# Kernel optimization log

Measured on AMD Instinct MI355X. Metric: run time of the kernel, lower is better.

Reference implementation:

```python
import jax, jax.numpy as jnp
import numpy as np

B, N, M, D = 8, 4096, 4096, 2


def setup_inputs() -> dict:
    key = jax.random.key(0)
    k1, k2, k3, k4 = jax.random.split(key, 4)
    return {
        "predicted_coords": jax.random.normal(k1, (B, N, D), dtype=jnp.float32),
        "predicted_points": jax.random.randint(k2, (B,), N // 2, N + 1, dtype=jnp.int32),
        "target_coords": jax.random.normal(k3, (B, M, D), dtype=jnp.float32),
        "target_points": jax.random.randint(k4, (B,), M // 2, M + 1, dtype=jnp.int32),
    }


def reference(predicted_coords, predicted_points, target_coords, target_points):
    # predicted_coords: [B, N, D], target_coords: [B, M, D]
    # predicted_points / target_points: [B] valid counts
    n = predicted_coords.shape[1]
    d = predicted_coords.shape[2]

    # points_loss = MSE(pred_counts/N, target_counts/N) over the batch
    points_loss = jnp.mean(
        (predicted_points.astype(jnp.float32) / n - target_points.astype(jnp.float32) / n) ** 2
    )

    # Batched 1-NN: squared pairwise distances [B, N, M], invalid targets masked to +inf.
    # (argmin of squared Euclidean == argmin of Euclidean, matching KDTree k=1.)
    d2 = jnp.sum((predicted_coords[:, :, None, :] - target_coords[:, None, :, :]) ** 2, axis=-1)
    tmask = jnp.arange(target_coords.shape[1])[None, :] < target_points[:, None]  # [B, M]
    d2 = jnp.where(tmask[:, None, :], d2, jnp.inf)
    idx = jnp.argmin(d2, axis=-1)  # [B, N]

    # Matched targets are detached in the original (numpy round-trip) -> stop_gradient.
    matched = jax.lax.stop_gradient(
        jnp.take_along_axis(target_coords, idx[:, :, None], axis=1)
    )  # [B, N, D]

    sq = jnp.sum((predicted_coords - matched) ** 2, axis=-1)  # [B, N]
    pmask = jnp.arange(predicted_coords.shape[1])[None, :] < predicted_points[:, None]  # [B, N]
    # Per-sample MSE over valid pred points (mean over count*D elements), then mean over batch.
    denom = predicted_points.astype(jnp.float32) * d
    coord_loss = jnp.mean(jnp.sum(jnp.where(pmask, sq, 0.0), axis=-1) / denom)

    total_loss = coord_loss + 0.1 * points_loss
    return (total_loss, coord_loss, points_loss)
```

## Files before the change

kernel.cpp:

```cpp
#include <hip/hip_runtime.h>
#include <math.h>

#define NB 8
#define NPTS 4096
#define MPTS 4096
#define CHUNK 64
#define NCHUNK (NPTS / CHUNK)
#define NWAVE 8
#define TQ (MPTS / NWAVE)

__device__ __forceinline__ float waveReduceSum(float v) {
#pragma unroll
    for (int off = 32; off > 0; off >>= 1)
        v += __shfl_down(v, off, 64);
    return v;
}

__global__ __launch_bounds__(NWAVE * 64) void nn_kernel(
    const float2* __restrict__ pred,
    const int* __restrict__ pcounts,
    const float2* __restrict__ tgt,
    const int* __restrict__ tcounts,
    float* __restrict__ partials)
{
    __shared__ float sx[MPTS];
    __shared__ float sy[MPTS];
    __shared__ float sc[MPTS];
    __shared__ float mnw[NWAVE][CHUNK];

    const int g = blockIdx.x;
    const int b = g >> 6;
    const int c = g & (NCHUNK - 1);
    const int w = threadIdx.x >> 6;
    const int lane = threadIdx.x & 63;

    const int tcount = tcounts[b];
    const int tstart = w * TQ;

    const float2* tsrc = tgt + (size_t)b * MPTS + tstart;
#pragma unroll
    for (int i = 0; i < TQ / 64; ++i) {
        float2 t = tsrc[i * 64 + lane];
        int idx = tstart + i * 64 + lane;
        sx[idx] = -2.0f * t.x;
        sy[idx] = -2.0f * t.y;
        sc[idx] = fmaf(t.x, t.x, t.y * t.y);
    }

    const float2 p = pred[(size_t)b * NPTS + c * CHUNK + lane];

    int tloc = min(tcount - tstart, TQ);
    if (tloc < 0) tloc = 0;

    float m0 = INFINITY, m1 = INFINITY, m2 = INFINITY, m3 = INFINITY;
    const float4* x4 = (const float4*)&sx[tstart];
    const float4* y4 = (const float4*)&sy[tstart];
    const float4* c4 = (const float4*)&sc[tstart];
    const int nt4 = tloc >> 2;
    for (int i = 0; i < nt4; ++i) {
        float4 xv = x4[i], yv = y4[i], cv = c4[i];
        m0 = fminf(m0, fmaf(p.y, yv.x, fmaf(p.x, xv.x, cv.x)));
        m1 = fminf(m1, fmaf(p.y, yv.y, fmaf(p.x, xv.y, cv.y)));
        m2 = fminf(m2, fmaf(p.y, yv.z, fmaf(p.x, xv.z, cv.z)));
        m3 = fminf(m3, fmaf(p.y, yv.w, fmaf(p.x, xv.w, cv.w)));
    }
    for (int m = nt4 * 4; m < tloc; ++m) {
        float v = fmaf(p.y, sy[tstart + m], fmaf(p.x, sx[tstart + m], sc[tstart + m]));
        m0 = fminf(m0, v);
    }
    mnw[w][lane] = fminf(fminf(m0, m1), fminf(m2, m3));
    __syncthreads();

    if (w == 0) {
        float mn = mnw[0][lane];
#pragma unroll
        for (int j = 1; j < NWAVE; ++j) mn = fminf(mn, mnw[j][lane]);
        float pp = fmaf(p.x, p.x, p.y * p.y);
        float v = (c * CHUNK + lane < pcounts[b]) ? (mn + pp) : 0.0f;
        v = waveReduceSum(v);
        if (lane == 0) partials[g] = v;
    }
}

__global__ __launch_bounds__(512) void final_kernel(
    const float* __restrict__ partials,
    const int* __restrict__ pcounts,
    const int* __restrict__ tcounts,
    float* __restrict__ out)
{
    __shared__ float bs[NB];
    const int w = threadIdx.x >> 6;
    const int lane = threadIdx.x & 63;
    float v = partials[w * NCHUNK + lane];
    v = waveReduceSum(v);
    if (lane == 0) bs[w] = v;
    __syncthreads();
    if (threadIdx.x == 0) {
        float coord = 0.0f, pts = 0.0f;
        for (int b = 0; b < NB; ++b) {
            coord += bs[b] / ((float)pcounts[b] * 2.0f);
            float d = ((float)pcounts[b] - (float)tcounts[b]) / (float)NPTS;
            pts += d * d;
        }
        coord *= (1.0f / NB);
        pts *= (1.0f / NB);
        out[0] = coord + 0.1f * pts;
        out[1] = coord;
        out[2] = pts;
    }
}

extern "C" void kernel_launch(void* const* d_in, const int* in_sizes, int n_in,
                              void* d_out, int out_size, void* d_ws, size_t ws_size,
                              hipStream_t stream) {
    const float2* pred    = (const float2*)d_in[0];
    const int*    pcounts = (const int*)d_in[1];
    const float2* tgt     = (const float2*)d_in[2];
    const int*    tcounts = (const int*)d_in[3];
    float* out = (float*)d_out;

    float* partials = (float*)d_ws;

    nn_kernel<<<NB * NCHUNK, NWAVE * 64, 0, stream>>>(
        pred, pcounts, tgt, tcounts, partials);
    final_kernel<<<1, 512, 0, stream>>>(partials, pcounts, tcounts, out);
}
```

Baseline: 20.33 us.

## Process two predictions per lane with packed FP32 math and 1024-thread blocks

Restructures the nearest-neighbour kernel so each lane handles two predicted points, reusing every loaded target pair. Inner-loop arithmetic uses v_pk_fma/v_pk_mul and v_min3. The target-norm array is no longer precomputed in shared memory; norms are recomputed per target, trading extra FMAs for less LDS traffic. Blocks grow to 1024 threads in 16 waves, halving the block count to 256, and the target load becomes vectorised float4. The final reduction is simplified to a single wave with shuffles.

```diff
diff --git a/kernel.cpp b/kernel.cpp
--- a/kernel.cpp
+++ b/kernel.cpp
@@ -4,10 +4,32 @@
 #define NB 8
 #define NPTS 4096
 #define MPTS 4096
-#define CHUNK 64
-#define NCHUNK (NPTS / CHUNK)
-#define NWAVE 8
-#define TQ (MPTS / NWAVE)
+#define BN (NB * NPTS)
+#define K1_THREADS 1024
+#define K1_WAVES 16
+#define SLICE (MPTS / K1_WAVES)
+#define P 2
+#define PPB (64 * P)
+#define NBLK (BN / PPB)
+#define BPB (NPTS / PPB)
+
+typedef float v2f __attribute__((ext_vector_type(2)));
+
+static __device__ __forceinline__ v2f pk_fma(v2f a, v2f b, v2f c) {
+    v2f d;
+    asm("v_pk_fma_f32 %0, %1, %2, %3" : "=v"(d) : "v"(a), "v"(b), "v"(c));
+    return d;
+}
+static __device__ __forceinline__ v2f pk_mul(v2f a, v2f b) {
+    v2f d;
+    asm("v_pk_mul_f32 %0, %1, %2" : "=v"(d) : "v"(a), "v"(b));
+    return d;
+}
+static __device__ __forceinline__ float min3f(float a, float b, float c) {
+    float d;
+    asm("v_min3_f32 %0, %1, %2, %3" : "=v"(d) : "v"(a), "v"(b), "v"(c));
+    return d;
+}
 
 __device__ __forceinline__ float waveReduceSum(float v) {
 #pragma unroll
@@ -16,7 +38,7 @@
     return v;
 }
 
-__global__ __launch_bounds__(NWAVE * 64) void nn_kernel(
+__global__ __launch_bounds__(K1_THREADS) void nn_kernel(
     const float2* __restrict__ pred,
     const int* __restrict__ pcounts,
     const float2* __restrict__ tgt,
@@ -25,83 +47,106 @@
 {
     __shared__ float sx[MPTS];
     __shared__ float sy[MPTS];
-    __shared__ float sc[MPTS];
-    __shared__ float mnw[NWAVE][CHUNK];
+    __shared__ float mnw[K1_WAVES][PPB];
+    __shared__ float wsum[2];
 
-    const int g = blockIdx.x;
-    const int b = g >> 6;
-    const int c = g & (NCHUNK - 1);
-    const int w = threadIdx.x >> 6;
-    const int lane = threadIdx.x & 63;
+    const int bid = blockIdx.x;
+    const int b = bid >> 5;
+    const int tid = threadIdx.x;
+    const int w = tid >> 6, lane = tid & 63;
+
+    {
+        const float4* t4 = (const float4*)(tgt + (size_t)b * MPTS);
+        float4 f0 = t4[tid];
+        float4 f1 = t4[tid + K1_THREADS];
+        *(v2f*)&sx[2 * tid] = (v2f){f0.x, f0.z};
+        *(v2f*)&sy[2 * tid] = (v2f){f0.y, f0.w};
+        *(v2f*)&sx[2 * (tid + K1_THREADS)] = (v2f){f1.x, f1.z};
+        *(v2f*)&sy[2 * (tid + K1_THREADS)] = (v2f){f1.y, f1.w};
+    }
+
+    const size_t pbase = (size_t)bid * PPB + lane;
+    const float2 p0 = pred[pbase];
+    const float2 p1 = pred[pbase + 64];
+    const v2f n2x0 = {-2.0f * p0.x, -2.0f * p0.x};
+    const v2f n2y0 = {-2.0f * p0.y, -2.0f * p0.y};
+    const v2f n2x1 = {-2.0f * p1.x, -2.0f * p1.x};
+    const v2f n2y1 = {-2.0f * p1.y, -2.0f * p1.y};
 
     const int tcount = tcounts[b];
-    const int tstart = w * TQ;
-
-    const float2* tsrc = tgt + (size_t)b * MPTS + tstart;
-#pragma unroll
-    for (int i = 0; i < TQ / 64; ++i) {
-        float2 t = tsrc[i * 64 + lane];
-        int idx = tstart + i * 64 + lane;
-        sx[idx] = -2.0f * t.x;
-        sy[idx] = -2.0f * t.y;
-        sc[idx] = fmaf(t.x, t.x, t.y * t.y);
-    }
-
-    const float2 p = pred[(size_t)b * NPTS + c * CHUNK + lane];
-
-    int tloc = min(tcount - tstart, TQ);
+    const int pcount = pcounts[b];
+    const int tstart = w * SLICE;
+    int tloc = min(tcount - tstart, SLICE);
     if (tloc < 0) tloc = 0;
 
-    float m0 = INFINITY, m1 = INFINITY, m2 = INFINITY, m3 = INFINITY;
+    __syncthreads();
+
+    float a00 = INFINITY, a01 = INFINITY, a10 = INFINITY, a11 = INFINITY;
     const float4* x4 = (const float4*)&sx[tstart];
     const float4* y4 = (const float4*)&sy[tstart];
-    const float4* c4 = (const float4*)&sc[tstart];
     const int nt4 = tloc >> 2;
+#pragma unroll 2
     for (int i = 0; i < nt4; ++i) {
-        float4 xv = x4[i], yv = y4[i], cv = c4[i];
-        m0 = fminf(m0, fmaf(p.y, yv.x, fmaf(p.x, xv.x, cv.x)));
-        m1 = fminf(m1, fmaf(p.y, yv.y, fmaf(p.x, xv.y, cv.y)));
-        m2 = fminf(m2, fmaf(p.y, yv.z, fmaf(p.x, xv.z, cv.z)));
-        m3 = fminf(m3, fmaf(p.y, yv.w, fmaf(p.x, xv.w, cv.w)));
+        float4 xv = x4[i], yv = y4[i];
+        v2f x01 = {xv.x, xv.y}, x23 = {xv.z, xv.w};
+        v2f y01 = {yv.x, yv.y}, y23 = {yv.z, yv.w};
+        v2f c01 = pk_fma(x01, x01, pk_mul(y01, y01));
+        v2f c23 = pk_fma(x23, x23, pk_mul(y23, y23));
+        v2f t;
+        t = pk_fma(n2y0, y01, pk_fma(n2x0, x01, c01)); a00 = min3f(a00, t.x, t.y);
+        t = pk_fma(n2y0, y23, pk_fma(n2x0, x23, c23)); a01 = min3f(a01, t.x, t.y);
+        t = pk_fma(n2y1, y01, pk_fma(n2x1, x01, c01)); a10 = min3f(a10, t.x, t.y);
+        t = pk_fma(n2y1, y23, pk_fma(n2x1, x23, c23)); a11 = min3f(a11, t.x, t.y);
     }
     for (int m = nt4 * 4; m < tloc; ++m) {
-        float v = fmaf(p.y, sy[tstart + m], fmaf(p.x, sx[tstart + m], sc[tstart + m]));
-        m0 = fminf(m0, v);
+        float tx = sx[tstart + m], ty = sy[tstart + m];
+        float cc = fmaf(tx, tx, ty * ty);
+        a00 = fminf(a00, fmaf(n2y0.x, ty, fmaf(n2x0.x, tx, cc)));
+        a10 = fminf(a10, fmaf(n2y1.x, ty, fmaf(n2x1.x, tx, cc)));
     }
-    mnw[w][lane] = fminf(fminf(m0, m1), fminf(m2, m3));
+    mnw[w][lane] = fminf(a00, a01);
+    mnw[w][lane + 64] = fminf(a10, a11);
     __syncthreads();
 
-    if (w == 0) {
-        float mn = mnw[0][lane];
+    if (tid < PPB) {
+        float v = mnw[0][tid];
 #pragma unroll
-        for (int j = 1; j < NWAVE; ++j) mn = fminf(mn, mnw[j][lane]);
-        float pp = fmaf(p.x, p.x, p.y * p.y);
-        float v = (c * CHUNK + lane < pcounts[b]) ? (mn + pp) : 0.0f;
+        for (int j = 1; j < K1_WAVES; ++j) v = fminf(v, mnw[j][tid]);
+        const size_t pg = (size_t)bid * PPB + tid;
+        float2 pp = pred[pg];
+        v += fmaf(pp.x, pp.x, pp.y * pp.y);
+        const int n = (int)(pg & (NPTS - 1));
+        v = (n < pcount) ? v : 0.0f;
         v = waveReduceSum(v);
-        if (lane == 0) partials[g] = v;
+        if ((tid & 63) == 0) wsum[tid >> 6] = v;
     }
+    __syncthreads();
+    if (tid == 0) partials[bid] = wsum[0] + wsum[1];
 }
 
-__global__ __launch_bounds__(512) void final_kernel(
+__global__ __launch_bounds__(64) void final_kernel(
     const float* __restrict__ partials,
     const int* __restrict__ pcounts,
     const int* __restrict__ tcounts,
     float* __restrict__ out)
 {
-    __shared__ float bs[NB];
-    const int w = threadIdx.x >> 6;
-    const int lane = threadIdx.x & 63;
-    float v = partials[w * NCHUNK + lane];
-    v = waveReduceSum(v);
-    if (lane == 0) bs[w] = v;
-    __syncthreads();
-    if (threadIdx.x == 0) {
-        float coord = 0.0f, pts = 0.0f;
-        for (int b = 0; b < NB; ++b) {
-            coord += bs[b] / ((float)pcounts[b] * 2.0f);
-            float d = ((float)pcounts[b] - (float)tcounts[b]) / (float)NPTS;
-            pts += d * d;
-        }
+    const int lane = threadIdx.x;
+    float coord_l = 0.0f, pts_l = 0.0f;
+    if (lane < NB) {
+        float s = 0.0f;
+        for (int k = 0; k < BPB; ++k) s += partials[lane * BPB + k];
+        float pc = (float)pcounts[lane];
+        coord_l = s / (pc * 2.0f);
+        float d = (pc - (float)tcounts[lane]) * (1.0f / NPTS);
+        pts_l = d * d;
+    }
+    float coord = 0.0f, pts = 0.0f;
+#pragma unroll
+    for (int b2 = 0; b2 < NB; ++b2) {
+        coord += __shfl(coord_l, b2, 64);
+        pts   += __shfl(pts_l, b2, 64);
+    }
+    if (lane == 0) {
         coord *= (1.0f / NB);
         pts *= (1.0f / NB);
         out[0] = coord + 0.1f * pts;
@@ -121,7 +166,6 @@
 
     float* partials = (float*)d_ws;
 
-    nn_kernel<<<NB * NCHUNK, NWAVE * 64, 0, stream>>>(
-        pred, pcounts, tgt, tcounts, partials);
-    final_kernel<<<1, 512, 0, stream>>>(partials, pcounts, tcounts, out);
+    nn_kernel<<<NBLK, K1_THREADS, 0, stream>>>(pred, pcounts, tgt, tcounts, partials);
+    final_kernel<<<1, 64, 0, stream>>>(partials, pcounts, tcounts, out);
 }
```

Result: faster. 19.26 us (-5.2%).
